# Performance work log

Measured on AMD Instinct MI355X. Metric: run time of the kernel, lower is better.

The kernel has to match this reference:

```python
import jax, jax.numpy as jnp
import numpy as np

D_MODEL = 1024
N_HEADS = 16
D_HEAD = D_MODEL // N_HEADS
D_FF = 4096
BATCH = 2
SEQ = 2048
EPS = 1e-5


def setup_inputs() -> dict:
    key = jax.random.key(0)
    ks = jax.random.split(key, 8)
    s = 0.02
    x = jax.random.normal(ks[0], (BATCH, SEQ, D_MODEL), dtype=jnp.float32)
    # Per-head projection weights, stacked: [H, d_head, d_model] (torch Linear stores (out,in))
    wq = jax.random.normal(ks[1], (N_HEADS, D_HEAD, D_MODEL), dtype=jnp.float32) * s
    wk = jax.random.normal(ks[2], (N_HEADS, D_HEAD, D_MODEL), dtype=jnp.float32) * s
    wv = jax.random.normal(ks[3], (N_HEADS, D_HEAD, D_MODEL), dtype=jnp.float32) * s
    wo = jax.random.normal(ks[4], (D_MODEL, D_MODEL), dtype=jnp.float32) * s
    w1 = jax.random.normal(ks[5], (D_FF, D_MODEL), dtype=jnp.float32) * s
    w2 = jax.random.normal(ks[6], (D_MODEL, D_FF), dtype=jnp.float32) * s
    ln1_g = jnp.ones((D_MODEL,), jnp.float32)
    ln1_b = jnp.zeros((D_MODEL,), jnp.float32)
    ln2_g = jnp.ones((D_MODEL,), jnp.float32)
    ln2_b = jnp.zeros((D_MODEL,), jnp.float32)
    return {"x": x, "wq": wq, "wk": wk, "wv": wv, "wo": wo,
            "w1": w1, "w2": w2, "ln1_g": ln1_g, "ln1_b": ln1_b,
            "ln2_g": ln2_g, "ln2_b": ln2_b}


def _layer_norm(x, g, b):
    mu = jnp.mean(x, axis=-1, keepdims=True)
    var = jnp.mean(jnp.square(x - mu), axis=-1, keepdims=True)
    return (x - mu) * jax.lax.rsqrt(var + EPS) * g + b


def _mha(h, wq, wk, wv, wo):
    # h: [b,s,d]; wq/wk/wv: [H,dh,d] -> q/k/v: [b,H,s,dh]
    q = jnp.einsum('bsd,hed->bhse', h, wq)
    k = jnp.einsum('bsd,hed->bhse', h, wk)
    v = jnp.einsum('bsd,hed->bhse', h, wv)
    scores = jnp.einsum('bhqe,bhke->bhqk', q, k) / jnp.sqrt(jnp.float32(D_HEAD))
    weights = jax.nn.softmax(scores, axis=-1)
    ctx = jnp.einsum('bhqk,bhke->bhqe', weights, v)  # [b,H,s,dh]
    # concat heads in order (head 0 first) -> [b,s,H*dh]
    concat = jnp.transpose(ctx, (0, 2, 1, 3)).reshape(h.shape[0], h.shape[1], D_MODEL)
    return concat @ wo.T


def reference(x, wq, wk, wv, wo, w1, w2, ln1_g, ln1_b, ln2_g, ln2_b):
    h = _layer_norm(x, ln1_g, ln1_b)
    attn_out = _mha(h, wq, wk, wv, wo)
    h2 = _layer_norm(x + attn_out, ln2_g, ln2_b)
    ff = jax.nn.gelu(h2 @ w1.T, approximate=False) @ w2.T
    return x + ff
```

## Files before the change

kernel.cpp:

```cpp
#include <hip/hip_runtime.h>
#include <hip/hip_bf16.h>
#include <math.h>

typedef __bf16 bf16_t;
typedef __bf16 bf16x8 __attribute__((ext_vector_type(8)));
typedef __bf16 bf16x4 __attribute__((ext_vector_type(4)));
typedef float f32x4 __attribute__((ext_vector_type(4)));
typedef unsigned int u32;
typedef u32 u32x2 __attribute__((ext_vector_type(2)));

#define DM 1024
#define SEQL 2048
#define NTOK 4096
#define QKVN 3072

__device__ __forceinline__ void gload_lds16(const bf16_t* g, bf16_t* l){
  __builtin_amdgcn_global_load_lds((const __attribute__((address_space(1))) void*)g,
                                   (__attribute__((address_space(3))) void*)l, 16, 0, 0);
}
__device__ __forceinline__ u32 ldsoff(const void* p){
  return (u32)(size_t)(__attribute__((address_space(3))) const void*)p;
}
__device__ __forceinline__ u32x2 tr64(u32 byte_off){
  u32x2 d;
  asm volatile("ds_read_b64_tr_b16 %0, %1" : "=v"(d) : "v"(byte_off));
  return d;
}
__device__ __forceinline__ u32 pack2(float a, float b){
  union{ __bf16 h[2]; u32 w; } z;
  z.h[0]=(__bf16)a; z.h[1]=(__bf16)b; return z.w;
}

__global__ __launch_bounds__(256) void cvt_kernel(const float* __restrict__ src,
    bf16_t* __restrict__ dst, int n)
{
  const int i = (blockIdx.x*256 + threadIdx.x)*4;
  if (i < n){
    const float4 v = *(const float4*)(src + i);
    bf16x4 o; o[0]=(__bf16)v.x; o[1]=(__bf16)v.y; o[2]=(__bf16)v.z; o[3]=(__bf16)v.w;
    *(bf16x4*)(dst + i) = o;
  }
}

__global__ __launch_bounds__(256) void ln_kernel(const float* __restrict__ in,
    const float* __restrict__ g, const float* __restrict__ bta,
    bf16_t* __restrict__ outp)
{
  const int row = blockIdx.x;
  const int t = threadIdx.x;
  const float4 v = *(const float4*)(in + (size_t)row*DM + t*4);
  float s  = v.x+v.y+v.z+v.w;
  float sq = v.x*v.x+v.y*v.y+v.z*v.z+v.w*v.w;
  #pragma unroll
  for (int m=1;m<64;m<<=1){ s += __shfl_xor(s,m); sq += __shfl_xor(sq,m); }
  __shared__ float red[8];
  const int w = t>>6;
  if ((t&63)==0){ red[w]=s; red[4+w]=sq; }
  __syncthreads();
  s  = red[0]+red[1]+red[2]+red[3];
  sq = red[4]+red[5]+red[6]+red[7];
  const float mean = s*(1.f/DM);
  const float var  = sq*(1.f/DM) - mean*mean;
  const float rstd = rsqrtf(var + 1e-5f);
  const float4 gg = *(const float4*)(g + t*4);
  const float4 bb = *(const float4*)(bta + t*4);
  bf16x4 o;
  o[0]=(__bf16)((v.x-mean)*rstd*gg.x+bb.x);
  o[1]=(__bf16)((v.y-mean)*rstd*gg.y+bb.y);
  o[2]=(__bf16)((v.z-mean)*rstd*gg.z+bb.z);
  o[3]=(__bf16)((v.w-mean)*rstd*gg.w+bb.w);
  *(bf16x4*)(outp + (size_t)row*DM + t*4) = o;
}

template<int EPI>
__global__ __launch_bounds__(512, 2) void gemm256(
    const bf16_t* __restrict__ A, const bf16_t* __restrict__ Bw,
    void* __restrict__ Cout, int N, int K)
{
  constexpr int BK = 32;
  __shared__ __align__(16) char ldsb[3*32768];
  const int tid = threadIdx.x, lane = tid&63, wid = tid>>6;
  const int q16 = lane&15, g = lane>>4;
  const int wm = wid>>2, wn = wid&3;

  const int flat = blockIdx.y*gridDim.x + blockIdx.x;
  const int xcd = flat&7, j = flat>>3;
  const int NY = gridDim.y;
  const int jdiv = j/NY, jmod = j - jdiv*NY;
  const int bm = (xcd*2 + jdiv)*256, bn = jmod*256;

  int mloc, kloc;
  {
    const u32 L = tid*16;
    const u32 logical = L ^ (((L>>9)&1)<<5);
    mloc = (int)((logical>>10)*16 + ((logical&1023)>>6));
    kloc = (int)((logical&63)>>1);
  }
  const bf16_t* asrc[2]; const bf16_t* bsrc[2];
  #pragma unroll
  for (int ht=0; ht<2; ht++){
    asrc[ht] = A  + (size_t)(bm + ht*128 + mloc)*K + kloc;
    bsrc[ht] = Bw + (size_t)(bn + ht*128 + mloc)*K + kloc;
  }
  const u32 laneOff = ((u32)(q16*64 + g*16)) ^ ((u32)(q16&8)<<2);

  f32x4 acc[8][4] = {};

  auto stageA = [&](int buf, int ht, int k0){
    gload_lds16(asrc[ht] + k0, (bf16_t*)(ldsb + buf*32768 + ht*8192 + tid*16));
  };
  auto stageB = [&](int buf, int ht, int k0){
    gload_lds16(bsrc[ht] + k0, (bf16_t*)(ldsb + buf*32768 + 16384 + ht*8192 + tid*16));
  };

  stageA(0,0,0); stageA(0,1,0); stageB(0,0,0); stageB(0,1,0);
  stageA(1,0,BK); stageA(1,1,BK); stageB(1,0,BK); stageB(1,1,BK);
  asm volatile("s_waitcnt vmcnt(4)" ::: "memory");
  __builtin_amdgcn_s_barrier();

  const int NT = K/BK;
  int bcur = 0;
  for (int kt=0; kt<NT; kt++){
    const int bstg = (bcur >= 1) ? bcur-1 : bcur+2;
    const char* Ab = ldsb + bcur*32768 + wm*8192;
    const char* Bb = ldsb + bcur*32768 + 16384 + (wn>>1)*8192;
    const bool sOK = (kt+2 < NT);
    const int k0s = (kt+2)*BK;
    bf16x8 bv[4];
    #pragma unroll
    for (int p=0; p<2; p++){
      bf16x8 av[4];
      #pragma unroll
      for (int jx=0;jx<4;jx++)
        av[jx] = *(const bf16x8*)(Ab + ((p*4+jx)<<10) + laneOff);
      if (p==0){
        #pragma unroll
        for (int jx=0;jx<4;jx++)
          bv[jx] = *(const bf16x8*)(Bb + ((((wn&1)*4)+jx)<<10) + laneOff);
      }
      if (sOK){
        if (p==0){ stageA(bstg,0,k0s); stageA(bstg,1,k0s); }
        else     { stageB(bstg,0,k0s); stageB(bstg,1,k0s); }
      }
      asm volatile("s_barrier" ::: "memory");
      __builtin_amdgcn_s_setprio(1);
      #pragma unroll
      for (int jx=0;jx<4;jx++)
        #pragma unroll
        for (int j2=0;j2<4;j2++)
          acc[p*4+jx][j2] = __builtin_amdgcn_mfma_f32_16x16x32_bf16(av[jx], bv[j2], acc[p*4+jx][j2], 0,0,0);
      __builtin_amdgcn_s_setprio(0);
      if (p==1){
        if (sOK) asm volatile("s_waitcnt vmcnt(4)" ::: "memory");
        else     asm volatile("s_waitcnt vmcnt(0)" ::: "memory");
      }
      asm volatile("s_barrier" ::: "memory");
    }
    bcur = (bcur==2)?0:bcur+1;
  }

  #pragma unroll
  for (int fm=0; fm<8; fm++)
    #pragma unroll
    for (int fn=0; fn<4; fn++)
      #pragma unroll
      for (int i=0; i<4; i++){
        const int r = bm + wm*128 + fm*16 + g*4 + i;
        const int c = bn + wn*64 + fn*16 + q16;
        const size_t idx = (size_t)r*N + c;
        const float vv = acc[fm][fn][i];
        if constexpr (EPI==0){
          ((bf16_t*)Cout)[idx] = (__bf16)vv;
        } else {
          const float ge = 0.5f*vv*(1.0f + erff(vv*0.70710678118654752f));
          ((bf16_t*)Cout)[idx] = (__bf16)ge;
        }
      }
}

template<int EPI, int BM, int MAP>
__global__ __launch_bounds__(256) void gemm_bt(
    const bf16_t* __restrict__ A, const bf16_t* __restrict__ Bw,
    void* __restrict__ Cout, const float* __restrict__ X,
    int N, int K)
{
  constexpr int BN=128, BK=32;
  constexpr int FM = BM/32;
  __shared__ __align__(16) bf16_t As[2][BM][BK];
  __shared__ __align__(16) bf16_t Bs[2][BN][BK];
  const int tid = threadIdx.x, lane = tid&63, wid = tid>>6;

  int bxi, byi;
  if constexpr (MAP==0){ bxi = blockIdx.x; byi = blockIdx.y; }
  else {
    const int flat = blockIdx.y*gridDim.x + blockIdx.x;
    const int xcd = flat&7, j = flat>>3;
    if constexpr (MAP==1){ bxi = (xcd<<3) + (j>>3); byi = j&7; }
    else                 { bxi = ((xcd>>2)<<5) + (j>>1); byi = ((xcd&3)<<1) + (j&1); }
  }
  const int bm = bxi*BM, bn = byi*BN;
  const int wr = (wid>>1)*(BM/2), wc = (wid&1)*64;
  const int grow = lane>>2, gk = (lane&3)*8;

  f32x4 acc[FM][4] = {};

  const int NT = K/BK;
  auto stage = [&](int buf, int k0){
    #pragma unroll
    for (int c = wid; c < BM/16; c += 4)
      gload_lds16(A + (size_t)(bm + c*16 + grow)*K + k0 + gk, &As[buf][c*16][0]);
    #pragma unroll
    for (int c = wid; c < 8; c += 4)
      gload_lds16(Bw + (size_t)(bn + c*16 + grow)*K + k0 + gk, &Bs[buf][c*16][0]);
  };

  stage(0, 0);
  for (int t=0; t<NT; t++){
    __syncthreads();
    if (t+1 < NT) stage((t+1)&1, (t+1)*BK);
    const int b = t&1;
    bf16x8 af[FM], bfv[4];
    #pragma unroll
    for (int fm=0; fm<FM; fm++)
      af[fm] = *(const bf16x8*)&As[b][wr+fm*16+(lane&15)][(lane>>4)*8];
    #pragma unroll
    for (int fn=0; fn<4; fn++)
      bfv[fn] = *(const bf16x8*)&Bs[b][wc+fn*16+(lane&15)][(lane>>4)*8];
    #pragma unroll
    for (int fm=0; fm<FM; fm++)
      #pragma unroll
      for (int fn=0; fn<4; fn++)
        acc[fm][fn] = __builtin_amdgcn_mfma_f32_16x16x32_bf16(af[fm], bfv[fn], acc[fm][fn], 0, 0, 0);
  }

  #pragma unroll
  for (int fm=0; fm<FM; fm++)
    #pragma unroll
    for (int fn=0; fn<4; fn++)
      #pragma unroll
      for (int i=0; i<4; i++){
        const int r = bm + wr + fm*16 + (lane>>4)*4 + i;
        const int c = bn + wc + fn*16 + (lane&15);
        const size_t idx = (size_t)r*N + c;
        const float vv = acc[fm][fn][i];
        if constexpr (EPI==1){
          ((float*)Cout)[idx] = X[idx] + vv;
        } else {
          ((bf16_t*)Cout)[idx] = (__bf16)vv;
        }
      }
}

__global__ __launch_bounds__(512, 4) void attn_kernel(
    const bf16_t* __restrict__ QKV, bf16_t* __restrict__ Ctx)
{
  __shared__ __align__(16) bf16_t Ks[2][64*64];
  __shared__ __align__(16) bf16_t Vs[2][16*4*72];
  const int tid = threadIdx.x, lane = tid&63, w = tid>>6;
  const int g = lane>>4, q16 = lane&15;
  const int bh = blockIdx.y, b = bh>>4, h = bh&15;
  const int qr0 = blockIdx.x*128 + w*16;
  const size_t tok0 = (size_t)b*SEQL;
  const int ch0 = h*64;

  bf16x8 aq[2];
  #pragma unroll
  for (int ks=0; ks<2; ks++){
    bf16x8 t = *(const bf16x8*)(QKV + (tok0+qr0+q16)*QKVN + ch0 + ks*32 + g*8);
    #pragma unroll
    for (int jx=0;jx<8;jx++) t[jx] = (__bf16)((float)t[jx]*0.125f);
    aq[ks] = t;
  }

  const int srow = tid>>3, sc8 = (tid&7)*8;
  const bf16_t* kptr = QKV + (tok0+srow)*QKVN + 1024 + ch0 + sc8;
  const bf16_t* vptr = kptr + 1024;
  const int kwoff = srow*64 + (sc8 ^ ((srow&7)<<3));
  const int vwoff = ((srow>>2)*4 + (sc8>>4))*72 + (srow&3)*16 + (sc8&15);

  float mrun = -1e30f, lrun = 0.f;
  f32x4 o[4] = {};

  bf16x8 kreg = *(const bf16x8*)kptr;
  bf16x8 vreg = *(const bf16x8*)vptr;
  *(bf16x8*)&Ks[0][kwoff] = kreg;
  *(bf16x8*)&Vs[0][vwoff] = vreg;
  kreg = *(const bf16x8*)(kptr + (size_t)64*QKVN);
  vreg = *(const bf16x8*)(vptr + (size_t)64*QKVN);

  const int NT = SEQL/64;
  for (int t=0; t<NT; t++){
    __syncthreads();
    if (t+1 < NT){
      *(bf16x8*)&Ks[(t+1)&1][kwoff] = kreg;
      *(bf16x8*)&Vs[(t+1)&1][vwoff] = vreg;
      if (t+2 < NT){
        kreg = *(const bf16x8*)(kptr + (size_t)(t+2)*64*QKVN);
        vreg = *(const bf16x8*)(vptr + (size_t)(t+2)*64*QKVN);
      }
    }
    const bf16_t* ksb = Ks[t&1];
    const u32 vs0 = ldsoff(&Vs[t&1][0]);

    f32x4 s[4] = {};
    #pragma unroll
    for (int ks=0; ks<2; ks++){
      #pragma unroll
      for (int fn=0; fn<4; fn++){
        const int r = fn*16 + q16;
        const int ce = ks*32 + g*8;
        bf16x8 bk = *(const bf16x8*)&ksb[r*64 + (ce ^ ((r&7)<<3))];
        s[fn] = __builtin_amdgcn_mfma_f32_16x16x32_bf16(bk, aq[ks], s[fn], 0, 0, 0);
      }
    }

    float m0 = fmaxf(fmaxf(s[0][0],s[0][1]), fmaxf(s[0][2],s[0][3]));
    float m1 = fmaxf(fmaxf(s[1][0],s[1][1]), fmaxf(s[1][2],s[1][3]));
    float m2 = fmaxf(fmaxf(s[2][0],s[2][1]), fmaxf(s[2][2],s[2][3]));
    float m3 = fmaxf(fmaxf(s[3][0],s[3][1]), fmaxf(s[3][2],s[3][3]));
    float mx = fmaxf(fmaxf(m0,m1), fmaxf(m2,m3));
    mx = fmaxf(mx, __shfl_xor(mx,16));
    mx = fmaxf(mx, __shfl_xor(mx,32));

    if (!__all(mx <= mrun + 8.0f)){
      const float mnew = fmaxf(mrun, mx);
      const float alpha = __expf(mrun - mnew);
      #pragma unroll
      for (int i=0;i<4;i++){
        const float ai = __shfl(alpha, g*4+i);
        o[0][i]*=ai; o[1][i]*=ai; o[2][i]*=ai; o[3][i]*=ai;
      }
      lrun *= alpha;
      mrun = mnew;
    }

    float rs = 0.f;
    u32 u[4][2];
    #pragma unroll
    for (int fn=0; fn<4; fn++){
      const float e0=__expf(s[fn][0]-mrun), e1=__expf(s[fn][1]-mrun);
      const float e2=__expf(s[fn][2]-mrun), e3=__expf(s[fn][3]-mrun);
      rs += (e0+e1)+(e2+e3);
      u[fn][0] = pack2(e0,e1);
      u[fn][1] = pack2(e2,e3);
    }
    rs += __shfl_xor(rs,16);
    rs += __shfl_xor(rs,32);
    lrun += rs;

    #pragma unroll
    for (int ks=0; ks<2; ks++){
      u32x2 vlo[4], vhi[4];
      #pragma unroll
      for (int ne=0; ne<4; ne++){
        const u32 vb = vs0 + (u32)((((ks*8 + 2*g)*4 + ne)*72 + q16)*2);
        vlo[ne] = tr64(vb);
        vhi[ne] = tr64(vb + 576);
      }
      union { u32 wd[4]; bf16x8 v; } pa;
      #pragma unroll
      for (int jj=0; jj<4; jj++){
        const int src = q16 + ((((g&1)<<1) + (jj>>1))<<4);
        const u32 a0 = (u32)__shfl((int)u[2*ks  ][jj&1], src);
        const u32 a1 = (u32)__shfl((int)u[2*ks+1][jj&1], src);
        pa.wd[jj] = (g&2) ? a1 : a0;
      }
      asm volatile("s_waitcnt lgkmcnt(0)" ::: "memory");
      __builtin_amdgcn_sched_barrier(0);
      union { u32x2 u2[2]; bf16x8 v; } cc;
      #pragma unroll
      for (int ne=0; ne<4; ne++){
        cc.u2[0]=vlo[ne]; cc.u2[1]=vhi[ne];
        o[ne] = __builtin_amdgcn_mfma_f32_16x16x32_bf16(pa.v, cc.v, o[ne], 0, 0, 0);
      }
    }
  }

  const float rl = 1.0f/lrun;
  #pragma unroll
  for (int i=0; i<4; i++){
    const float ri = __shfl(rl, g*4+i);
    #pragma unroll
    for (int ne=0; ne<4; ne++){
      const int r = qr0 + g*4 + i;
      Ctx[(tok0+r)*DM + ch0 + ne*16 + q16] = (__bf16)(o[ne][i]*ri);
    }
  }
}

extern "C" void kernel_launch(void* const* d_in, const int* in_sizes, int n_in,
                              void* d_out, int out_size, void* d_ws, size_t ws_size,
                              hipStream_t stream)
{
  (void)in_sizes; (void)n_in; (void)out_size; (void)ws_size;
  const float* x  = (const float*)d_in[0];
  const float* wq = (const float*)d_in[1];
  const float* wk = (const float*)d_in[2];
  const float* wv = (const float*)d_in[3];
  const float* wo = (const float*)d_in[4];
  const float* w1 = (const float*)d_in[5];
  const float* w2 = (const float*)d_in[6];
  const float* g1 = (const float*)d_in[7];
  const float* b1 = (const float*)d_in[8];
  const float* g2 = (const float*)d_in[9];
  const float* b2 = (const float*)d_in[10];
  float* out = (float*)d_out;
  char* ws = (char*)d_ws;
  const size_t MB = 1024ull*1024ull;

  bf16_t* wqkv_b = (bf16_t*)(ws);
  bf16_t* wo_b   = (bf16_t*)(ws + 6*MB);
  bf16_t* w1_b   = (bf16_t*)(ws + 8*MB);
  bf16_t* w2_b   = (bf16_t*)(ws + 16*MB);
  bf16_t* h1     = (bf16_t*)(ws + 24*MB);
  bf16_t* qkv    = (bf16_t*)(ws + 32*MB);
  bf16_t* ctx    = (bf16_t*)(ws + 56*MB);
  float*  res2   = (float*)(ws + 64*MB);
  bf16_t* h2     = h1;
  bf16_t* ffm    = (bf16_t*)(ws + 32*MB);

  cvt_kernel<<<1024, 256, 0, stream>>>(wq, wqkv_b,             1024*1024);
  cvt_kernel<<<1024, 256, 0, stream>>>(wk, wqkv_b + 1024*1024, 1024*1024);
  cvt_kernel<<<1024, 256, 0, stream>>>(wv, wqkv_b + 2048*1024, 1024*1024);
  cvt_kernel<<<1024, 256, 0, stream>>>(wo, wo_b, 1024*1024);
  cvt_kernel<<<4096, 256, 0, stream>>>(w1, w1_b, 4096*1024);
  cvt_kernel<<<4096, 256, 0, stream>>>(w2, w2_b, 4096*1024);

  ln_kernel<<<NTOK, 256, 0, stream>>>(x, g1, b1, h1);
  gemm256<0><<<dim3(16, 12), 512, 0, stream>>>(h1, wqkv_b, (void*)qkv, QKVN, 1024);
  attn_kernel<<<dim3(16, 32), 512, 0, stream>>>(qkv, ctx);
  gemm_bt<1,64,1><<<dim3(64, 8), 256, 0, stream>>>(ctx, wo_b, (void*)res2, x, 1024, 1024);
  ln_kernel<<<NTOK, 256, 0, stream>>>(res2, g2, b2, h2);
  gemm256<2><<<dim3(16, 16), 512, 0, stream>>>(h2, w1_b, (void*)ffm, 4096, 1024);
  gemm_bt<1,64,2><<<dim3(64, 8), 256, 0, stream>>>(ffm, w2_b, (void*)out, x, 1024, 4096);
}
```

Before: 285.8 us.

## Replace residual GEMMs with 128x128 triple-buffered swizzled-LDS kernel

Replaces the 64x128 double-buffered gemm_bt used for the Wo and W2 residual projections with a new 128x128 tile kernel run by 512 threads. It uses a three-stage LDS ring filled by direct global-to-LDS loads, XOR-swizzled LDS offsets to avoid bank conflicts, and split barriers with s_setprio around the MFMA groups. Loads are interleaved with compute so the next tile arrives while the current one is multiplied. The grid drops to 256 blocks with an XCD-aware mapping, which means fewer blocks to spread over the CUs in exchange for more reuse per block.

Result: faster. 261.0 us (-8.7%).

```diff
diff --git a/kernel.cpp b/kernel.cpp
--- a/kernel.cpp
+++ b/kernel.cpp
@@ -178,76 +178,97 @@
       }
 }
 
-template<int EPI, int BM, int MAP>
-__global__ __launch_bounds__(256) void gemm_bt(
+__global__ __launch_bounds__(512, 2) void gemm128(
     const bf16_t* __restrict__ A, const bf16_t* __restrict__ Bw,
-    void* __restrict__ Cout, const float* __restrict__ X,
+    float* __restrict__ Cout, const float* __restrict__ X,
     int N, int K)
 {
-  constexpr int BN=128, BK=32;
-  constexpr int FM = BM/32;
-  __shared__ __align__(16) bf16_t As[2][BM][BK];
-  __shared__ __align__(16) bf16_t Bs[2][BN][BK];
+  constexpr int BK = 32;
+  __shared__ __align__(16) char ldsb[3*16384];
   const int tid = threadIdx.x, lane = tid&63, wid = tid>>6;
-
-  int bxi, byi;
-  if constexpr (MAP==0){ bxi = blockIdx.x; byi = blockIdx.y; }
-  else {
-    const int flat = blockIdx.y*gridDim.x + blockIdx.x;
-    const int xcd = flat&7, j = flat>>3;
-    if constexpr (MAP==1){ bxi = (xcd<<3) + (j>>3); byi = j&7; }
-    else                 { bxi = ((xcd>>2)<<5) + (j>>1); byi = ((xcd&3)<<1) + (j&1); }
-  }
-  const int bm = bxi*BM, bn = byi*BN;
-  const int wr = (wid>>1)*(BM/2), wc = (wid&1)*64;
-  const int grow = lane>>2, gk = (lane&3)*8;
-
-  f32x4 acc[FM][4] = {};
+  const int q16 = lane&15, g = lane>>4;
+  const int wm = wid>>2, wn = wid&3;
+
+  const int flat = blockIdx.y*gridDim.x + blockIdx.x;
+  const int xcd = flat&7, j = flat>>3;
+  const int bm = ((xcd<<2) + (j>>3))*128, bn = (j&7)*128;
+
+  int mloc, kloc;
+  {
+    const u32 L = tid*16;
+    const u32 logical = L ^ (((L>>9)&1)<<5);
+    mloc = (int)((logical>>10)*16 + ((logical&1023)>>6));
+    kloc = (int)((logical&63)>>1);
+  }
+  const bf16_t* asrc = A  + (size_t)(bm + mloc)*K + kloc;
+  const bf16_t* bsrc = Bw + (size_t)(bn + mloc)*K + kloc;
+  const u32 laneOff = ((u32)(q16*64 + g*16)) ^ ((u32)(q16&8)<<2);
+
+  f32x4 acc[4][2] = {};
+
+  auto stageA = [&](int buf, int k0){
+    gload_lds16(asrc + k0, (bf16_t*)(ldsb + buf*16384 + tid*16));
+  };
+  auto stageB = [&](int buf, int k0){
+    gload_lds16(bsrc + k0, (bf16_t*)(ldsb + buf*16384 + 8192 + tid*16));
+  };
+
+  stageA(0,0); stageB(0,0);
+  stageA(1,BK); stageB(1,BK);
+  asm volatile("s_waitcnt vmcnt(2)" ::: "memory");
+  __builtin_amdgcn_s_barrier();
 
   const int NT = K/BK;
-  auto stage = [&](int buf, int k0){
-    #pragma unroll
-    for (int c = wid; c < BM/16; c += 4)
-      gload_lds16(A + (size_t)(bm + c*16 + grow)*K + k0 + gk, &As[buf][c*16][0]);
-    #pragma unroll
-    for (int c = wid; c < 8; c += 4)
-      gload_lds16(Bw + (size_t)(bn + c*16 + grow)*K + k0 + gk, &Bs[buf][c*16][0]);
-  };
-
-  stage(0, 0);
-  for (int t=0; t<NT; t++){
-    __syncthreads();
-    if (t+1 < NT) stage((t+1)&1, (t+1)*BK);
-    const int b = t&1;
-    bf16x8 af[FM], bfv[4];
-    #pragma unroll
-    for (int fm=0; fm<FM; fm++)
-      af[fm] = *(const bf16x8*)&As[b][wr+fm*16+(lane&15)][(lane>>4)*8];
-    #pragma unroll
-    for (int fn=0; fn<4; fn++)
-      bfv[fn] = *(const bf16x8*)&Bs[b][wc+fn*16+(lane&15)][(lane>>4)*8];
-    #pragma unroll
-    for (int fm=0; fm<FM; fm++)
-      #pragma unroll
-      for (int fn=0; fn<4; fn++)
-        acc[fm][fn] = __builtin_amdgcn_mfma_f32_16x16x32_bf16(af[fm], bfv[fn], acc[fm][fn], 0, 0, 0);
-  }
-
-  #pragma unroll
-  for (int fm=0; fm<FM; fm++)
-    #pragma unroll
-    for (int fn=0; fn<4; fn++)
+  int bcur = 0;
+  for (int kt=0; kt<NT; kt++){
+    const int bstg = (bcur >= 1) ? bcur-1 : bcur+2;
+    const char* Ab = ldsb + bcur*16384 + wm*4096;
+    const char* Bb = ldsb + bcur*16384 + 8192 + wn*2048;
+    const bool sOK = (kt+2 < NT);
+    const int k0s = (kt+2)*BK;
+    bf16x8 bv[2];
+    #pragma unroll
+    for (int p=0; p<2; p++){
+      bf16x8 av[2];
+      #pragma unroll
+      for (int jx=0;jx<2;jx++)
+        av[jx] = *(const bf16x8*)(Ab + ((p*2+jx)<<10) + laneOff);
+      if (p==0){
+        #pragma unroll
+        for (int jx=0;jx<2;jx++)
+          bv[jx] = *(const bf16x8*)(Bb + (jx<<10) + laneOff);
+      }
+      if (sOK){
+        if (p==0) stageA(bstg,k0s);
+        else      stageB(bstg,k0s);
+      }
+      asm volatile("s_barrier" ::: "memory");
+      __builtin_amdgcn_s_setprio(1);
+      #pragma unroll
+      for (int jx=0;jx<2;jx++)
+        #pragma unroll
+        for (int j2=0;j2<2;j2++)
+          acc[p*2+jx][j2] = __builtin_amdgcn_mfma_f32_16x16x32_bf16(av[jx], bv[j2], acc[p*2+jx][j2], 0,0,0);
+      __builtin_amdgcn_s_setprio(0);
+      if (p==1){
+        if (sOK) asm volatile("s_waitcnt vmcnt(2)" ::: "memory");
+        else     asm volatile("s_waitcnt vmcnt(0)" ::: "memory");
+      }
+      asm volatile("s_barrier" ::: "memory");
+    }
+    bcur = (bcur==2)?0:bcur+1;
+  }
+
+  #pragma unroll
+  for (int fm=0; fm<4; fm++)
+    #pragma unroll
+    for (int fn=0; fn<2; fn++)
       #pragma unroll
       for (int i=0; i<4; i++){
-        const int r = bm + wr + fm*16 + (lane>>4)*4 + i;
-        const int c = bn + wc + fn*16 + (lane&15);
+        const int r = bm + wm*64 + fm*16 + g*4 + i;
+        const int c = bn + wn*32 + fn*16 + q16;
         const size_t idx = (size_t)r*N + c;
-        const float vv = acc[fm][fn][i];
-        if constexpr (EPI==1){
-          ((float*)Cout)[idx] = X[idx] + vv;
-        } else {
-          ((bf16_t*)Cout)[idx] = (__bf16)vv;
-        }
+        Cout[idx] = X[idx] + acc[fm][fn][i];
       }
 }
 
@@ -429,8 +450,8 @@
   ln_kernel<<<NTOK, 256, 0, stream>>>(x, g1, b1, h1);
   gemm256<0><<<dim3(16, 12), 512, 0, stream>>>(h1, wqkv_b, (void*)qkv, QKVN, 1024);
   attn_kernel<<<dim3(16, 32), 512, 0, stream>>>(qkv, ctx);
-  gemm_bt<1,64,1><<<dim3(64, 8), 256, 0, stream>>>(ctx, wo_b, (void*)res2, x, 1024, 1024);
+  gemm128<<<dim3(32, 8), 512, 0, stream>>>(ctx, wo_b, res2, x, 1024, 1024);
   ln_kernel<<<NTOK, 256, 0, stream>>>(res2, g2, b2, h2);
   gemm256<2><<<dim3(16, 16), 512, 0, stream>>>(h2, w1_b, (void*)ffm, 4096, 1024);
-  gemm_bt<1,64,2><<<dim3(64, 8), 256, 0, stream>>>(ffm, w2_b, (void*)out, x, 1024, 4096);
-}
+  gemm128<<<dim3(32, 8), 512, 0, stream>>>(ffm, w2_b, out, x, 1024, 4096);
+}
```
